# Optimization experiments

Hardware: AMD Instinct MI355X
Metric: run time of the kernel (lower is better)

Reference implementation:

```python
import jax, jax.numpy as jnp
import numpy as np

B, T, C, H = 512, 256, 512, 4
HS = C // H          # head_size = 128
FF = 4 * C           # ffn_fanout * n_embd = 2048
NF = 2               # n_ffn dual FFN branches
EPS = 1e-8


def setup_inputs() -> dict:
    key = jax.random.key(0)
    ks = jax.random.split(key, 12)
    s = 0.02
    return {
        "x": jax.random.normal(ks[0], (B, T, C), jnp.float32),
        "Wq": jax.random.normal(ks[1], (H, C, HS), jnp.float32) * s,
        "Wk": jax.random.normal(ks[2], (H, C, HS), jnp.float32) * s,
        "bk": jax.random.normal(ks[3], (H, HS), jnp.float32) * s,
        "Wv": jax.random.normal(ks[4], (H, C, HS), jnp.float32) * s,
        "Wproj": jax.random.normal(ks[5], (C, C), jnp.float32) * s,
        "bproj": jax.random.normal(ks[6], (C,), jnp.float32) * s,
        "w1": jnp.ones((1,), jnp.float32),
        "w2": jnp.ones((1,), jnp.float32),
        "Wi": jax.random.normal(ks[7], (NF, C, FF), jnp.float32) * s,
        "Wo": jax.random.normal(ks[8], (NF, FF, C), jnp.float32) * s,
    }


def _rmsnorm(v, w):
    # MyNorm: scalar weight * x * rsqrt(mean(x^2, -1) + eps)
    return w * v * jax.lax.rsqrt(jnp.mean(v * v, axis=-1, keepdims=True) + EPS)


def reference(x, Wq, Wk, bk, Wv, Wproj, bproj, w1, w2, Wi, Wo):
    Bc, Tc, Cc = x.shape
    h = _rmsnorm(x, w1)
    # per-head projections (key has bias; query/value do not)
    q = jnp.einsum("btc,hcd->bhtd", h, Wq)
    k = jnp.einsum("btc,hcd->bhtd", h, Wk) + bk[None, :, None, :]
    v = jnp.einsum("btc,hcd->bhtd", h, Wv)
    # NOTE: original scales by full channel dim C**-0.5, not head_size
    scale = Cc ** (-0.5)
    wei = jnp.einsum("bhtd,bhsd->bhts", q, k) * scale
    causal = jnp.tril(jnp.ones((Tc, Tc), bool))
    wei = jnp.where(causal[None, None], wei, -jnp.inf)
    wei = jax.nn.softmax(wei, axis=-1)  # dropout: identity (inference)
    attn = jnp.einsum("bhts,bhsd->bhtd", wei, v)
    attn = attn.transpose(0, 2, 1, 3).reshape(Bc, Tc, Cc)
    x = x + attn @ Wproj + bproj  # dropout before proj: identity
    x = _rmsnorm(x, w2)
    # dual-branch FFN, averaged (exact GELU, as torch nn.GELU default)
    hmid = jax.nn.gelu(jnp.einsum("btc,ncf->nbtf", x, Wi), approximate=False)
    ff = jnp.mean(jnp.einsum("nbtf,nfc->nbtc", hmid, Wo), axis=0)
    return x + ff
```

## Files before the change

### kernel.cpp

```cpp
#include <hip/hip_runtime.h>
#include <cstdint>
#include <cstddef>

#define TOKENS 131072
#define B_BATCH 512
#define T_SEQ 256
#define C_DIM 512
#define H_HEADS 4
#define HS_DIM 128
#define FF_DIM 2048
#define EPS_RMS 1e-8f
#define SM_SCALE 0.044194173824159216f

typedef short bf16x8 __attribute__((ext_vector_type(8)));
typedef float f32x4 __attribute__((ext_vector_type(4)));
typedef unsigned short ushort_t;

__device__ __forceinline__ ushort_t f2bf(float f) {
    uint32_t u = __builtin_bit_cast(uint32_t, f);
    u += 0x7FFFu + ((u >> 16) & 1u);
    return (ushort_t)(u >> 16);
}

__device__ __forceinline__ float gelu_f(float x) {
    float u = 0.7978845608028654f * x + 0.035677408136300125f * (x * x * x);
    float e = __expf(2.0f * u);
    float t = 1.0f - 2.0f / (1.0f + e);
    return 0.5f * x * (1.0f + t);
}

__device__ __forceinline__ void stage8k(ushort_t* lds, const ushort_t* g) {
    __builtin_amdgcn_global_load_lds(
        (const __attribute__((address_space(1))) uint32_t*)g,
        (__attribute__((address_space(3))) uint32_t*)lds,
        16, 0, 0);
}

__global__ void prep_qkv(const float* __restrict__ Wq, const float* __restrict__ Wk,
                         const float* __restrict__ Wv, ushort_t* __restrict__ WqkvT) {
    int idx = blockIdx.x * 256 + threadIdx.x;
    if (idx >= 1536 * 512) return;
    int n = idx >> 9;
    int k = idx & 511;
    int h = (n & 511) >> 7;
    int d = n & 127;
    float v;
    size_t s = ((size_t)h * 512 + k) * 128 + d;
    if (n < 512)       v = Wq[s];
    else if (n < 1024) v = Wk[s];
    else               v = Wv[s];
    WqkvT[idx] = f2bf(v);
}

__global__ void prep_bias(const float* __restrict__ bk, float* __restrict__ bias1536) {
    int n = blockIdx.x * 256 + threadIdx.x;
    if (n >= 1536) return;
    bias1536[n] = (n >= 512 && n < 1024) ? bk[n - 512] : 0.0f;
}

__global__ void prep_proj(const float* __restrict__ Wproj, ushort_t* __restrict__ WprojT) {
    int idx = blockIdx.x * 256 + threadIdx.x;
    if (idx >= 512 * 512) return;
    int n = idx >> 9, k = idx & 511;
    WprojT[idx] = f2bf(Wproj[(size_t)k * 512 + n]);
}

__global__ void prep_wi(const float* __restrict__ Wi, ushort_t* __restrict__ WiT) {
    int idx = blockIdx.x * 256 + threadIdx.x;
    if (idx >= 2 * 2048 * 512) return;
    int b = idx >> 20;
    int rem = idx & 1048575;
    int f = rem >> 9, c = rem & 511;
    WiT[idx] = f2bf(Wi[((size_t)b * 512 + c) * 2048 + f]);
}

__global__ void prep_wo(const float* __restrict__ Wo, ushort_t* __restrict__ WoT2) {
    int idx = blockIdx.x * 256 + threadIdx.x;
    if (idx >= 512 * 4096) return;
    int c  = idx >> 12;
    int n2 = idx & 4095;
    int br = n2 >> 11;
    int f  = n2 & 2047;
    WoT2[idx] = f2bf(0.5f * Wo[(((size_t)br * 2048 + f) * 512) + c]);
}

template<int WRITE_F32>
__global__ __launch_bounds__(256) void rmsnorm_kernel(const float* __restrict__ in,
                                                      const float* __restrict__ wptr,
                                                      ushort_t* __restrict__ outb,
                                                      float* outf) {
    const int lane = threadIdx.x & 63;
    const int wave = threadIdx.x >> 6;
    const size_t token = (size_t)blockIdx.x * 4 + wave;
    const float* row = in + token * 512;
    float4 v0 = *(const float4*)(row + lane * 8);
    float4 v1 = *(const float4*)(row + lane * 8 + 4);
    float ss = v0.x*v0.x + v0.y*v0.y + v0.z*v0.z + v0.w*v0.w
             + v1.x*v1.x + v1.y*v1.y + v1.z*v1.z + v1.w*v1.w;
    #pragma unroll
    for (int d = 32; d; d >>= 1) ss += __shfl_xor(ss, d);
    float scale = wptr[0] * rsqrtf(ss * (1.0f / 512.0f) + EPS_RMS);
    float vals[8] = {v0.x, v0.y, v0.z, v0.w, v1.x, v1.y, v1.z, v1.w};
    union { ushort_t us[8]; uint4 u4; } pk;
    #pragma unroll
    for (int i = 0; i < 8; i++) pk.us[i] = f2bf(vals[i] * scale);
    *(uint4*)(outb + token * 512 + lane * 8) = pk.u4;
    if (WRITE_F32) {
        float4 o0 = make_float4(v0.x*scale, v0.y*scale, v0.z*scale, v0.w*scale);
        float4 o1 = make_float4(v1.x*scale, v1.y*scale, v1.z*scale, v1.w*scale);
        *(float4*)(outf + token * 512 + lane * 8)     = o0;
        *(float4*)(outf + token * 512 + lane * 8 + 4) = o1;
    }
}

template<int MODE>
__global__ __launch_bounds__(512) void gemm256(
    const ushort_t* __restrict__ A, const ushort_t* __restrict__ Bt,
    float* Cf, ushort_t* __restrict__ Cb,
    const float* __restrict__ bias, const float* __restrict__ X,
    int N, int K)
{
    __shared__ __align__(16) ushort_t S[2][2][256 * 64];
    const int tid  = threadIdx.x;
    const int lane = tid & 63;
    const int wave = tid >> 6;
    const int wm = wave >> 2;
    const int wn = wave & 3;

    const int nwg  = (int)gridDim.x;
    const int orig = (int)blockIdx.x;
    const int wgid = (orig & 7) * (nwg >> 3) + (orig >> 3);
    const int gx   = N >> 8;
    const int bm = (wgid / gx) << 8;
    const int bn = (wgid % gx) << 8;

    const int NT = K >> 6;

    const int sx = (((lane & 7) ^ (lane >> 3)) << 3);

    auto stA = [&](int dbuf, int part, int ts) {
        int tc = ts < NT ? ts : NT - 1;
        #pragma unroll
        for (int i = 0; i < 2; i++) {
            int rbase = i * 128 + part * 64 + wave * 8;
            stage8k(&S[dbuf][0][rbase * 64],
                    A + (size_t)(bm + rbase + (lane >> 3)) * K + tc * 64 + sx);
        }
    };
    auto stB = [&](int dbuf, int part, int ts) {
        int tc = ts < NT ? ts : NT - 1;
        #pragma unroll
        for (int i = 0; i < 2; i++) {
            int rbase = i * 128 + (wave >> 2) * 64 + part * 32 + (wave & 3) * 8;
            stage8k(&S[dbuf][1][rbase * 64],
                    Bt + (size_t)(bn + rbase + (lane >> 3)) * K + tc * 64 + sx);
        }
    };

    const int r16 = lane & 15;
    const int l7  = lane & 7;
    const int q   = lane >> 4;
    const int ge0 = ((q)     ^ l7) << 3;
    const int ge1 = ((4 + q) ^ l7) << 3;

    f32x4 acc[8][4] = {};
    bf16x8 a[4][2], bA[2][2], bB[2][2];

#define LDA(BUF, MH) { _Pragma("unroll") for (int mf = 0; mf < 4; mf++) { \
    int R = wm * 128 + (MH) * 64 + mf * 16 + r16; \
    a[mf][0] = *(const bf16x8*)&S[BUF][0][R * 64 + ge0]; \
    a[mf][1] = *(const bf16x8*)&S[BUF][0][R * 64 + ge1]; } }
#define LDB(BUF, NH, breg) { _Pragma("unroll") for (int nf = 0; nf < 2; nf++) { \
    int R = wn * 64 + (NH) * 32 + nf * 16 + r16; \
    breg[nf][0] = *(const bf16x8*)&S[BUF][1][R * 64 + ge0]; \
    breg[nf][1] = *(const bf16x8*)&S[BUF][1][R * 64 + ge1]; } }
#define MM(MH, NH, breg) { __builtin_amdgcn_s_setprio(1); \
    _Pragma("unroll") for (int mf = 0; mf < 4; mf++) \
    _Pragma("unroll") for (int nf = 0; nf < 2; nf++) { \
        f32x4 t0 = __builtin_amdgcn_mfma_f32_16x16x32_bf16(a[mf][0], breg[nf][0], acc[(MH)*4+mf][(NH)*2+nf], 0, 0, 0); \
        acc[(MH)*4+mf][(NH)*2+nf] = __builtin_amdgcn_mfma_f32_16x16x32_bf16(a[mf][1], breg[nf][1], t0, 0, 0, 0); } \
    __builtin_amdgcn_s_setprio(0); }
#define BAR    __builtin_amdgcn_s_barrier()
#define FEN    asm volatile("" ::: "memory")
#define FENV   asm volatile("s_waitcnt vmcnt(4)" ::: "memory")

    stA(0, 0, 0); stA(0, 1, 0); stB(0, 0, 0); stB(0, 1, 0);
    stA(1, 0, 1); stB(1, 1, 1);
    FENV;
    BAR;

    const int NI = NT >> 1;
    for (int I = 0; I < NI; ++I) {
        const int t = 2 * I;
        LDA(0, 0); LDB(0, 0, bA);  stA(1, 1, t + 1);  BAR; FEN;  MM(0, 0, bA); BAR;
        LDB(0, 1, bB);             stB(1, 0, t + 1);  BAR; FEN;  MM(0, 1, bB); BAR;
        LDA(0, 1);                 stA(0, 0, t + 2);  BAR; FEN;  MM(1, 1, bB); BAR;
                                   stB(0, 1, t + 2);  BAR; FENV; MM(1, 0, bA); BAR;
        LDA(1, 0); LDB(1, 0, bA);  stA(0, 1, t + 2);  BAR; FEN;  MM(0, 0, bA); BAR;
        LDB(1, 1, bB);             stB(0, 0, t + 2);  BAR; FEN;  MM(0, 1, bB); BAR;
        LDA(1, 1);                 stA(1, 0, t + 3);  BAR; FEN;  MM(1, 1, bB); BAR;
                                   stB(1, 1, t + 3);  BAR; FENV; MM(1, 0, bA); BAR;
    }
#undef LDA
#undef LDB
#undef MM
#undef BAR
#undef FEN
#undef FENV

    #pragma unroll
    for (int mf = 0; mf < 8; mf++) {
        #pragma unroll
        for (int nf = 0; nf < 4; nf++) {
            #pragma unroll
            for (int j = 0; j < 4; j++) {
                int r = bm + wm * 128 + mf * 16 + (lane >> 4) * 4 + j;
                int c = bn + wn * 64 + nf * 16 + r16;
                float v = acc[mf][nf][j];
                size_t idx = (size_t)r * N + c;
                if (MODE == 0)      { Cb[idx] = f2bf(v + bias[c]); }
                else if (MODE == 1) { Cf[idx] = v + bias[c] + X[idx]; }
                else if (MODE == 2) { Cb[idx] = f2bf(gelu_f(v)); }
                else                { Cf[idx] = X[idx] + v; }
            }
        }
    }
}

__global__ __launch_bounds__(256) void attn_kernel(const ushort_t* __restrict__ QKV,
                                                   ushort_t* __restrict__ Ao) {
    __shared__ __align__(16) ushort_t Ks[32 * 136];
    __shared__ __align__(16) ushort_t VsT[128 * 40];
    __shared__ __align__(16) ushort_t Ps[4][16 * 40];
    const int tid  = threadIdx.x;
    const int lane = tid & 63;
    const int wave = tid >> 6;
    const int qtile = blockIdx.x;
    const int bh = blockIdx.y;
    const int b = bh >> 2;
    const int h = bh & 3;
    const int qb = qtile * 64;
    const int q0 = qb + wave * 16;
    const size_t baseTok = (size_t)b * T_SEQ;

    bf16x8 qf[4];
    {
        const ushort_t* qrow = QKV + (baseTok + q0 + (lane & 15)) * 1536 + h * 128 + (lane >> 4) * 8;
        #pragma unroll
        for (int dc = 0; dc < 4; dc++)
            qf[dc] = *(const bf16x8*)(qrow + dc * 32);
    }

    float m_run[4], l_run[4];
    f32x4 o[8];
    #pragma unroll
    for (int j = 0; j < 4; j++) { m_run[j] = -INFINITY; l_run[j] = 0.0f; }
    #pragma unroll
    for (int nt = 0; nt < 8; nt++) o[nt] = f32x4{0.f, 0.f, 0.f, 0.f};

    const int nchunks = qtile * 2 + 2;
    for (int kc = 0; kc < nchunks; kc++) {
        const int kbase = kc * 32;
        __syncthreads();
        #pragma unroll
        for (int r = 0; r < 2; r++) {
            int li = r * 256 + tid;
            int row = li >> 4;
            int c8 = (li & 15) * 8;
            size_t g = (baseTok + kbase + row) * 1536;
            uint4 vk = *(const uint4*)(QKV + g + 512 + h * 128 + c8);
            *(uint4*)(&Ks[row * 136 + c8]) = vk;
            uint4 vv = *(const uint4*)(QKV + g + 1024 + h * 128 + c8);
            ushort_t* pv = (ushort_t*)&vv;
            #pragma unroll
            for (int jj = 0; jj < 8; jj++)
                VsT[(c8 + jj) * 40 + row] = pv[jj];
        }
        __syncthreads();

        if (q0 + 15 >= kbase) {
            f32x4 s0 = {0.f,0.f,0.f,0.f}, s1 = {0.f,0.f,0.f,0.f};
            #pragma unroll
            for (int dc = 0; dc < 4; dc++) {
                bf16x8 kf0 = *(const bf16x8*)(&Ks[(lane & 15) * 136 + dc * 32 + (lane >> 4) * 8]);
                bf16x8 kf1 = *(const bf16x8*)(&Ks[(16 + (lane & 15)) * 136 + dc * 32 + (lane >> 4) * 8]);
                s0 = __builtin_amdgcn_mfma_f32_16x16x32_bf16(qf[dc], kf0, s0, 0, 0, 0);
                s1 = __builtin_amdgcn_mfma_f32_16x16x32_bf16(qf[dc], kf1, s1, 0, 0, 0);
            }
            const int key0 = kbase + (lane & 15);
            const int key1 = key0 + 16;
            float p0[4], p1[4], alpha[4];
            #pragma unroll
            for (int j = 0; j < 4; j++) {
                int qrow = q0 + (lane >> 4) * 4 + j;
                float sv0 = (key0 <= qrow) ? s0[j] * SM_SCALE : -INFINITY;
                float sv1 = (key1 <= qrow) ? s1[j] * SM_SCALE : -INFINITY;
                float mx = fmaxf(sv0, sv1);
                #pragma unroll
                for (int d = 1; d < 16; d <<= 1) mx = fmaxf(mx, __shfl_xor(mx, d));
                float mnew = fmaxf(m_run[j], mx);
                float aa = expf(m_run[j] - mnew);
                p0[j] = expf(sv0 - mnew);
                p1[j] = expf(sv1 - mnew);
                float rs = p0[j] + p1[j];
                #pragma unroll
                for (int d = 1; d < 16; d <<= 1) rs += __shfl_xor(rs, d);
                l_run[j] = l_run[j] * aa + rs;
                m_run[j] = mnew;
                alpha[j] = aa;
            }
            #pragma unroll
            for (int nt = 0; nt < 8; nt++)
                #pragma unroll
                for (int j = 0; j < 4; j++) o[nt][j] *= alpha[j];
            #pragma unroll
            for (int j = 0; j < 4; j++) {
                int rloc = (lane >> 4) * 4 + j;
                Ps[wave][rloc * 40 + (lane & 15)]      = f2bf(p0[j]);
                Ps[wave][rloc * 40 + 16 + (lane & 15)] = f2bf(p1[j]);
            }
            bf16x8 pa = *(const bf16x8*)(&Ps[wave][(lane & 15) * 40 + (lane >> 4) * 8]);
            #pragma unroll
            for (int nt = 0; nt < 8; nt++) {
                bf16x8 vf = *(const bf16x8*)(&VsT[(nt * 16 + (lane & 15)) * 40 + (lane >> 4) * 8]);
                o[nt] = __builtin_amdgcn_mfma_f32_16x16x32_bf16(pa, vf, o[nt], 0, 0, 0);
            }
        }
    }

    #pragma unroll
    for (int j = 0; j < 4; j++) {
        float inv = 1.0f / l_run[j];
        size_t row = baseTok + q0 + (lane >> 4) * 4 + j;
        #pragma unroll
        for (int nt = 0; nt < 8; nt++)
            Ao[row * 512 + h * 128 + nt * 16 + (lane & 15)] = f2bf(o[nt][j] * inv);
    }
}

extern "C" void kernel_launch(void* const* d_in, const int* in_sizes, int n_in,
                              void* d_out, int out_size, void* d_ws, size_t ws_size,
                              hipStream_t stream) {
    const float* x     = (const float*)d_in[0];
    const float* Wq    = (const float*)d_in[1];
    const float* Wk    = (const float*)d_in[2];
    const float* bk    = (const float*)d_in[3];
    const float* Wv    = (const float*)d_in[4];
    const float* Wproj = (const float*)d_in[5];
    const float* bproj = (const float*)d_in[6];
    const float* w1    = (const float*)d_in[7];
    const float* w2    = (const float*)d_in[8];
    const float* Wi    = (const float*)d_in[9];
    const float* Wo    = (const float*)d_in[10];
    float* out = (float*)d_out;
    (void)in_sizes; (void)n_in; (void)out_size;

    char* ws = (char*)d_ws;
    size_t off = 0;
    auto alloc = [&](size_t bytes) -> void* {
        void* p = ws + off;
        off += (bytes + 255) & ~(size_t)255;
        return p;
    };
    ushort_t* WqkvT    = (ushort_t*)alloc((size_t)1536 * 512 * 2);
    float*    bias1536 = (float*)   alloc((size_t)1536 * 4);
    ushort_t* WprojT   = (ushort_t*)alloc((size_t)512 * 512 * 2);
    ushort_t* WiT      = (ushort_t*)alloc((size_t)4096 * 512 * 2);
    ushort_t* WoT2     = (ushort_t*)alloc((size_t)512 * 4096 * 2);
    const size_t weightBytes = off;

    int nchunks = 1;
    while (nchunks < 64) {
        size_t Mc = (size_t)TOKENS / nchunks;
        size_t need = weightBytes + Mc * 512 * 2 + Mc * 4096 * 2 + 4096;
        if (need <= ws_size) break;
        nchunks *= 2;
    }
    const size_t Mc = (size_t)TOKENS / nchunks;
    const int    nbChunk = B_BATCH / nchunks;

    ushort_t* hb  = (ushort_t*)alloc(Mc * 512 * 2);
    ushort_t* big = (ushort_t*)alloc(Mc * 4096 * 2);

    prep_qkv <<<(1536 * 512 + 255) / 256, 256, 0, stream>>>(Wq, Wk, Wv, WqkvT);
    prep_bias<<<6, 256, 0, stream>>>(bk, bias1536);
    prep_proj<<<1024, 256, 0, stream>>>(Wproj, WprojT);
    prep_wi  <<<8192, 256, 0, stream>>>(Wi, WiT);
    prep_wo  <<<8192, 256, 0, stream>>>(Wo, WoT2);

    for (int ck = 0; ck < nchunks; ck++) {
        const size_t t0 = (size_t)ck * Mc;
        const float* xC   = x + t0 * 512;
        float*       zC   = out + t0 * 512;
        const int    Mi   = (int)Mc;
        const int    mt   = Mi / 256;

        rmsnorm_kernel<0><<<Mi / 4, 256, 0, stream>>>(xC, w1, hb, nullptr);
        gemm256<0><<<mt * 6, 512, 0, stream>>>(
            hb, WqkvT, nullptr, big, bias1536, nullptr, 1536, 512);
        attn_kernel<<<dim3(T_SEQ / 64, nbChunk * H_HEADS), 256, 0, stream>>>(big, hb);
        gemm256<1><<<mt * 2, 512, 0, stream>>>(
            hb, WprojT, zC, nullptr, bproj, xC, 512, 512);
        rmsnorm_kernel<1><<<Mi / 4, 256, 0, stream>>>(zC, w2, hb, zC);
        gemm256<2><<<mt * 16, 512, 0, stream>>>(
            hb, WiT, nullptr, big, nullptr, nullptr, 4096, 512);
        gemm256<3><<<mt * 2, 512, 0, stream>>>(
            big, WoT2, zC, nullptr, nullptr, zC, 512, 4096);
    }
}
```

Before: 2.706 ms.

## Load GEMM A operand directly from global into registers, stage only B in LDS

The 256x256 GEMM kernel no longer stages the A tile through shared memory. Each wave loads its A fragments straight from global memory into double-buffered register sets (aP/aQ), while only B is staged into LDS with a simplified two-phase pipeline per K step. This halves LDS footprint and LDS traffic and cuts the number of barriers per iteration. In exchange it greatly increases VGPR pressure (two sets of 8x2 A fragments plus the accumulators), relies on launch_bounds(512,1), and the direct A global loads are 16-byte scattered rows with no LDS reuse across the wn waves, so A global traffic is duplicated fourfold.

New measurement: 10.76 ms. 298% more time.

```diff
diff --git a/kernel.cpp b/kernel.cpp
--- a/kernel.cpp
+++ b/kernel.cpp
@@ -114,13 +114,13 @@
 }
 
 template<int MODE>
-__global__ __launch_bounds__(512) void gemm256(
+__global__ __launch_bounds__(512, 1) void gemm256(
     const ushort_t* __restrict__ A, const ushort_t* __restrict__ Bt,
     float* Cf, ushort_t* __restrict__ Cb,
     const float* __restrict__ bias, const float* __restrict__ X,
     int N, int K)
 {
-    __shared__ __align__(16) ushort_t S[2][2][256 * 64];
+    __shared__ __align__(16) ushort_t S[2][256 * 64];
     const int tid  = threadIdx.x;
     const int lane = tid & 63;
     const int wave = tid >> 6;
@@ -137,22 +137,12 @@
     const int NT = K >> 6;
 
     const int sx = (((lane & 7) ^ (lane >> 3)) << 3);
-
-    auto stA = [&](int dbuf, int part, int ts) {
+    auto stB = [&](int dbuf, int ts) {
         int tc = ts < NT ? ts : NT - 1;
         #pragma unroll
-        for (int i = 0; i < 2; i++) {
-            int rbase = i * 128 + part * 64 + wave * 8;
-            stage8k(&S[dbuf][0][rbase * 64],
-                    A + (size_t)(bm + rbase + (lane >> 3)) * K + tc * 64 + sx);
-        }
-    };
-    auto stB = [&](int dbuf, int part, int ts) {
-        int tc = ts < NT ? ts : NT - 1;
-        #pragma unroll
-        for (int i = 0; i < 2; i++) {
-            int rbase = i * 128 + (wave >> 2) * 64 + part * 32 + (wave & 3) * 8;
-            stage8k(&S[dbuf][1][rbase * 64],
+        for (int i = 0; i < 4; i++) {
+            int rbase = wave * 32 + i * 8;
+            stage8k(&S[dbuf][rbase * 64],
                     Bt + (size_t)(bn + rbase + (lane >> 3)) * K + tc * 64 + sx);
         }
     };
@@ -160,63 +150,70 @@
     const int r16 = lane & 15;
     const int l7  = lane & 7;
     const int q   = lane >> 4;
-    const int ge0 = ((q)     ^ l7) << 3;
+    const int ge0 = ((q) ^ l7) << 3;
     const int ge1 = ((4 + q) ^ l7) << 3;
 
+    const ushort_t* aptr[8];
+    #pragma unroll
+    for (int f = 0; f < 8; f++) {
+        int row = bm + wm * 128 + (f >> 2) * 64 + (f & 3) * 16 + r16;
+        aptr[f] = A + (size_t)row * K + q * 8;
+    }
+
     f32x4 acc[8][4] = {};
-    bf16x8 a[4][2], bA[2][2], bB[2][2];
-
-#define LDA(BUF, MH) { _Pragma("unroll") for (int mf = 0; mf < 4; mf++) { \
-    int R = wm * 128 + (MH) * 64 + mf * 16 + r16; \
-    a[mf][0] = *(const bf16x8*)&S[BUF][0][R * 64 + ge0]; \
-    a[mf][1] = *(const bf16x8*)&S[BUF][0][R * 64 + ge1]; } }
-#define LDB(BUF, NH, breg) { _Pragma("unroll") for (int nf = 0; nf < 2; nf++) { \
-    int R = wn * 64 + (NH) * 32 + nf * 16 + r16; \
-    breg[nf][0] = *(const bf16x8*)&S[BUF][1][R * 64 + ge0]; \
-    breg[nf][1] = *(const bf16x8*)&S[BUF][1][R * 64 + ge1]; } }
-#define MM(MH, NH, breg) { __builtin_amdgcn_s_setprio(1); \
-    _Pragma("unroll") for (int mf = 0; mf < 4; mf++) \
-    _Pragma("unroll") for (int nf = 0; nf < 2; nf++) { \
-        f32x4 t0 = __builtin_amdgcn_mfma_f32_16x16x32_bf16(a[mf][0], breg[nf][0], acc[(MH)*4+mf][(NH)*2+nf], 0, 0, 0); \
-        acc[(MH)*4+mf][(NH)*2+nf] = __builtin_amdgcn_mfma_f32_16x16x32_bf16(a[mf][1], breg[nf][1], t0, 0, 0, 0); } \
+    bf16x8 aP[8][2], aQ[8][2], b[4][2];
+
+#define LDA_SET(SET, TS) { int ko = (((TS) < NT ? (TS) : NT - 1) << 6); \
+    _Pragma("unroll") for (int f = 0; f < 8; f++) { \
+        SET[f][0] = *(const bf16x8*)(aptr[f] + ko); \
+        SET[f][1] = *(const bf16x8*)(aptr[f] + ko + 32); } }
+#define LDB_ALL(BUF) { _Pragma("unroll") for (int nf = 0; nf < 4; nf++) { \
+    int R = wn * 64 + nf * 16 + r16; \
+    b[nf][0] = *(const bf16x8*)&S[BUF][R * 64 + ge0]; \
+    b[nf][1] = *(const bf16x8*)&S[BUF][R * 64 + ge1]; } }
+#define MM_ALL(ASET) { __builtin_amdgcn_s_setprio(1); \
+    _Pragma("unroll") for (int f = 0; f < 8; f++) \
+    _Pragma("unroll") for (int nf = 0; nf < 4; nf++) { \
+        f32x4 t0 = __builtin_amdgcn_mfma_f32_16x16x32_bf16(ASET[f][0], b[nf][0], acc[f][nf], 0, 0, 0); \
+        acc[f][nf] = __builtin_amdgcn_mfma_f32_16x16x32_bf16(ASET[f][1], b[nf][1], t0, 0, 0, 0); } \
     __builtin_amdgcn_s_setprio(0); }
-#define BAR    __builtin_amdgcn_s_barrier()
-#define FEN    asm volatile("" ::: "memory")
-#define FENV   asm volatile("s_waitcnt vmcnt(4)" ::: "memory")
-
-    stA(0, 0, 0); stA(0, 1, 0); stB(0, 0, 0); stB(0, 1, 0);
-    stA(1, 0, 1); stB(1, 1, 1);
-    FENV;
-    BAR;
+#define BODY(T, BUF, ACUR, ANXT) { \
+    LDB_ALL(BUF); \
+    asm volatile("s_waitcnt lgkmcnt(0)" ::: "memory"); \
+    __builtin_amdgcn_s_barrier(); \
+    stB(BUF, (T) + 2); \
+    LDA_SET(ANXT, (T) + 1); \
+    MM_ALL(ACUR); \
+    asm volatile("s_waitcnt vmcnt(20)" ::: "memory"); \
+    __builtin_amdgcn_s_barrier(); }
+
+    stB(0, 0);
+    asm volatile("" ::: "memory");
+    LDA_SET(aP, 0);
+    stB(1, 1);
+    asm volatile("s_waitcnt vmcnt(20)" ::: "memory");
+    __builtin_amdgcn_s_barrier();
 
     const int NI = NT >> 1;
     for (int I = 0; I < NI; ++I) {
         const int t = 2 * I;
-        LDA(0, 0); LDB(0, 0, bA);  stA(1, 1, t + 1);  BAR; FEN;  MM(0, 0, bA); BAR;
-        LDB(0, 1, bB);             stB(1, 0, t + 1);  BAR; FEN;  MM(0, 1, bB); BAR;
-        LDA(0, 1);                 stA(0, 0, t + 2);  BAR; FEN;  MM(1, 1, bB); BAR;
-                                   stB(0, 1, t + 2);  BAR; FENV; MM(1, 0, bA); BAR;
-        LDA(1, 0); LDB(1, 0, bA);  stA(0, 1, t + 2);  BAR; FEN;  MM(0, 0, bA); BAR;
-        LDB(1, 1, bB);             stB(0, 0, t + 2);  BAR; FEN;  MM(0, 1, bB); BAR;
-        LDA(1, 1);                 stA(1, 0, t + 3);  BAR; FEN;  MM(1, 1, bB); BAR;
-                                   stB(1, 1, t + 3);  BAR; FENV; MM(1, 0, bA); BAR;
-    }
-#undef LDA
-#undef LDB
-#undef MM
-#undef BAR
-#undef FEN
-#undef FENV
-
-    #pragma unroll
-    for (int mf = 0; mf < 8; mf++) {
+        BODY(t,     0, aP, aQ);
+        BODY(t + 1, 1, aQ, aP);
+    }
+#undef LDA_SET
+#undef LDB_ALL
+#undef MM_ALL
+#undef BODY
+
+    #pragma unroll
+    for (int f = 0; f < 8; f++) {
         #pragma unroll
         for (int nf = 0; nf < 4; nf++) {
             #pragma unroll
             for (int j = 0; j < 4; j++) {
-                int r = bm + wm * 128 + mf * 16 + (lane >> 4) * 4 + j;
+                int r = bm + wm * 128 + (f >> 2) * 64 + (f & 3) * 16 + (lane >> 4) * 4 + j;
                 int c = bn + wn * 64 + nf * 16 + r16;
-                float v = acc[mf][nf][j];
+                float v = acc[f][nf][j];
                 size_t idx = (size_t)r * N + c;
                 if (MODE == 0)      { Cb[idx] = f2bf(v + bias[c]); }
                 else if (MODE == 1) { Cf[idx] = v + bias[c] + X[idx]; }
```
